# Optimization experiments

Measured on AMD Instinct MI355X. Metric: run time of the kernel, lower is better.

## Reference

```python
import jax, jax.numpy as jnp
import numpy as np

N = 20000   # nodes
E = 160000  # edges
IN = 16     # in_channels
H = 32      # hidden_channels
MID = 32    # edge-MLP hidden width


def setup_inputs() -> dict:
    key = jax.random.key(0)
    ks = jax.random.split(key, 18)
    s = 0.1  # param scale
    return {
        "x": jax.random.normal(ks[0], (N, IN), jnp.float32),
        "edge_index": jax.random.randint(ks[1], (2, E), 0, N, dtype=jnp.int64),
        "edge_weight": jax.random.uniform(ks[2], (E,), jnp.float32),
        # edge_net1: Linear(1,32) -> SiLU -> Linear(32, IN*H)
        "en1_w1": jax.random.normal(ks[3], (1, MID), jnp.float32) * s,
        "en1_b1": jax.random.normal(ks[4], (MID,), jnp.float32) * s,
        "en1_w2": jax.random.normal(ks[5], (MID, IN * H), jnp.float32) * s,
        "en1_b2": jax.random.normal(ks[6], (IN * H,), jnp.float32) * s,
        "root1": jax.random.normal(ks[7], (IN, H), jnp.float32) * s,
        "bias1": jax.random.normal(ks[8], (H,), jnp.float32) * s,
        # edge_net2: Linear(1,32) -> SiLU -> Linear(32, H*H)
        "en2_w1": jax.random.normal(ks[9], (1, MID), jnp.float32) * s,
        "en2_b1": jax.random.normal(ks[10], (MID,), jnp.float32) * s,
        "en2_w2": jax.random.normal(ks[11], (MID, H * H), jnp.float32) * s,
        "en2_b2": jax.random.normal(ks[12], (H * H,), jnp.float32) * s,
        "root2": jax.random.normal(ks[13], (H, H), jnp.float32) * s,
        "bias2": jax.random.normal(ks[14], (H,), jnp.float32) * s,
        "dec_w": jax.random.normal(ks[15], (H, 1), jnp.float32) * s,
        "dec_b": jax.random.normal(ks[16], (1,), jnp.float32) * s,
    }


def _nnconv(x, src, dst, inv_cnt, e, w1, b1, w2, b2, root, bias, cin, cout):
    # edge MLP -> per-edge [cin, cout] weight matrix
    h = jax.nn.silu(e @ w1 + b1)            # [E, MID]
    w = (h @ w2 + b2).reshape(-1, cin, cout)  # [E, cin, cout]
    msg = jnp.einsum('ei,eio->eo', x[src], w)  # per-edge matmul [E, cout]
    agg = jax.ops.segment_sum(msg, dst, num_segments=N) * inv_cnt  # scatter-mean
    return agg + x @ root + bias


def reference(x, edge_index, edge_weight,
              en1_w1, en1_b1, en1_w2, en1_b2, root1, bias1,
              en2_w1, en2_b1, en2_w2, en2_b2, root2, bias2,
              dec_w, dec_b):
    src, dst = edge_index[0], edge_index[1]
    e = edge_weight[:, None]  # [E, 1]
    cnt = jax.ops.segment_sum(jnp.ones((E,), x.dtype), dst, num_segments=N)
    inv_cnt = (1.0 / jnp.maximum(cnt, 1.0))[:, None]  # [N, 1]
    h = _nnconv(x, src, dst, inv_cnt, e, en1_w1, en1_b1, en1_w2, en1_b2, root1, bias1, IN, H)
    h = jax.nn.silu(h)
    h = _nnconv(h, src, dst, inv_cnt, e, en2_w1, en2_b1, en2_w2, en2_b2, root2, bias2, H, H)
    h = jax.nn.silu(h)
    out = h @ dec_w + dec_b  # [N, 1]
    return out[:, 0]
```

## Files before the change

### kernel.cpp

```cpp
#include <hip/hip_runtime.h>
#include <hip/hip_bf16.h>

#define NN 20000
#define EE 160000
#define HH 32
#define MIDD 32
#define NB 128
#define EPB 1250

typedef _Float16 f16x4 __attribute__((ext_vector_type(4)));
typedef _Float16 f16x8 __attribute__((ext_vector_type(8)));
typedef float f32x4 __attribute__((ext_vector_type(4)));

__device__ __forceinline__ float silu_f(float v) {
    return __fdividef(v, 1.0f + __expf(-v));
}

__device__ __forceinline__ void gload_lds_b32(const void* gsrc, void* ldst) {
    __builtin_amdgcn_global_load_lds(
        (const __attribute__((address_space(1))) void*)gsrc,
        (__attribute__((address_space(3))) void*)ldst, 4, 0, 0);
}

__global__ __launch_bounds__(256) void prep_kernel(
    const int* __restrict__ ei,
    const float* __restrict__ w2a, const float* __restrict__ b2a,
    const float* __restrict__ ra,
    const float* __restrict__ w2b, const float* __restrict__ b2b,
    const float* __restrict__ rb,
    const float* __restrict__ x,
    unsigned int* __restrict__ histG,
    _Float16* __restrict__ Wt1, _Float16* __restrict__ Wt2,
    _Float16* __restrict__ x16) {
    const int t = threadIdx.x;
    if (blockIdx.x < NB) {
        __shared__ unsigned int h2[NN / 2];
        for (int i = t; i < NN / 2; i += 256) h2[i] = 0u;
        __syncthreads();
        const int base = blockIdx.x * EPB;
        for (int e = base + t; e < base + EPB; e += 256) {
            int d = ei[EE + e];
            atomicAdd(&h2[d >> 1], 1u << ((d & 1) * 16));
        }
        __syncthreads();
        unsigned int* outp = histG + (size_t)blockIdx.x * NN;
        for (int n = t; n < NN; n += 256)
            outp[n] = (h2[n >> 1] >> ((n & 1) * 16)) & 0xFFFFu;
        return;
    }
    int idx = (blockIdx.x - NB) * 256 + t;
    if (idx < 17408) {
        int o = idx / 544, k = idx % 544;
        float v;
        if (k < 512) {
            int m = k & 31, i = k >> 5;
            v = w2a[m * 512 + i * 32 + o];
        } else if (k < 528) {
            v = b2a[(k - 512) * 32 + o];
        } else {
            v = ra[(k - 528) * 32 + o];
        }
        Wt1[o * 544 + k] = (_Float16)v;
    } else if (idx < 52224) {
        int j = idx - 17408;
        int o = j / 1088, k = j % 1088;
        float v;
        if (k < 1024) {
            int m = k & 31, i = k >> 5;
            v = w2b[m * 1024 + i * 32 + o];
        } else if (k < 1056) {
            v = b2b[(k - 1024) * 32 + o];
        } else {
            v = rb[(k - 1056) * 32 + o];
        }
        Wt2[o * 1088 + k] = (_Float16)v;
    } else if (idx < 52224 + NN * 16) {
        int j = idx - 52224;
        x16[j] = (_Float16)x[j];
    }
}

__global__ __launch_bounds__(256) void colscan_kernel(
    unsigned int* __restrict__ histG, int* __restrict__ cnt,
    float* __restrict__ invc) {
    const int n = blockIdx.x * 256 + threadIdx.x;
    if (n >= NN) return;
    unsigned int s = 0;
    #pragma unroll 4
    for (int b = 0; b < NB; ++b) {
        unsigned int v = histG[(size_t)b * NN + n];
        histG[(size_t)b * NN + n] = s;
        s += v;
    }
    cnt[n] = (int)s;
    invc[n] = 1.0f / fmaxf((float)s, 1.0f);
}

__global__ __launch_bounds__(1024) void scan_kernel(
    const int* __restrict__ cnt, int* __restrict__ off) {
    const int t = threadIdx.x;
    const int base = t * 20;
    __shared__ int wtot[16];

    int c[20];
    if (base + 20 <= NN) {
        const int4* p = (const int4*)(cnt + base);
        #pragma unroll
        for (int q = 0; q < 5; ++q) *(int4*)&c[4 * q] = p[q];
    } else {
        #pragma unroll
        for (int r = 0; r < 20; ++r) {
            int idx = base + r;
            c[r] = (idx < NN) ? cnt[idx] : 0;
        }
    }

    int loc[20];
    int s = 0;
    #pragma unroll
    for (int r = 0; r < 20; ++r) { loc[r] = s; s += c[r]; }

    const int lane = t & 63, wv = t >> 6;
    int incl = s;
    #pragma unroll
    for (int d2 = 1; d2 < 64; d2 <<= 1) {
        int u = __shfl_up(incl, d2);
        if (lane >= d2) incl += u;
    }
    if (lane == 63) wtot[wv] = incl;
    __syncthreads();
    int wbase = 0;
    for (int p2 = 0; p2 < wv; ++p2) wbase += wtot[p2];

    const int excl = wbase + incl - s;

    int o[20];
    #pragma unroll
    for (int r = 0; r < 20; ++r) o[r] = excl + loc[r];

    if (base + 20 <= NN) {
        #pragma unroll
        for (int q = 0; q < 5; ++q)
            ((int4*)(off + base))[q] = *(const int4*)&o[4 * q];
    } else {
        #pragma unroll
        for (int r = 0; r < 20; ++r) {
            int idx = base + r;
            if (idx < NN) off[idx] = o[r];
        }
    }
    if (t == 0) off[NN] = EE;
}

__global__ __launch_bounds__(256) void scatter2_kernel(
    const int* __restrict__ ei, const float* __restrict__ ewt,
    const int* __restrict__ off, const unsigned int* __restrict__ histG,
    int2* __restrict__ spair) {
    __shared__ unsigned int r2[NN / 2];
    const int t = threadIdx.x, b = blockIdx.x;
    for (int i = t; i < NN / 2; i += 256) r2[i] = 0u;
    __syncthreads();
    const int base = b * EPB;
    const unsigned int* hb = histG + (size_t)b * NN;
    for (int e = base + t; e < base + EPB; e += 256) {
        int d = ei[EE + e];
        unsigned int old = atomicAdd(&r2[d >> 1], 1u << ((d & 1) * 16));
        int rank = (int)((old >> ((d & 1) * 16)) & 0xFFFFu);
        int pos = off[d] + (int)hb[d] + rank;
        spair[pos] = make_int2(ei[e], __float_as_int(ewt[e]));
    }
}


template <int CIN, bool DECODE>
__global__ __launch_bounds__(512, 4) void fused_layer(
    const _Float16* __restrict__ xin16, const int* __restrict__ spair,
    const int* __restrict__ off, const float* __restrict__ invc,
    const float* __restrict__ w1, const float* __restrict__ b1,
    const _Float16* __restrict__ Wt, const float* __restrict__ bias,
    void* __restrict__ outp, const float* __restrict__ dw,
    const float* __restrict__ db) {
    constexpr int K = 34 * CIN;
    constexpr int LDK = K + 4;
    constexpr int steps = K / 32;
    constexpr int CAP = 192;
    constexpr int RPG = 128 / CIN;
    constexpr int LPR = CIN / 2;
    constexpr int NIH = CIN / 16;

    extern __shared__ char smem[];
    _Float16* Fl = (_Float16*)smem;
    char* poolb = smem + (size_t)16 * LDK * 2;
    int* Ps = (int*)poolb;
    _Float16* Xs = (_Float16*)(poolb + (2 * CAP + 64) * 4);
    _Float16* Hs = Xs + CAP * CIN;
    float* red = (float*)poolb;

    const int t = threadIdx.x;
    const int n0 = blockIdx.x * 16;
    const int lane = t & 63, w = t >> 6;
    const int col = lane & 15, g4 = (lane >> 4) * 4;

    const int E0 = off[n0], E1 = off[n0 + 16];
    const int L = E1 - E0;

    const int d0 = n0 + w * 2;
    const int e0l0 = off[d0] - E0;
    const int e1l0 = off[d0 + 1] - E0;
    const int e1l1 = off[d0 + 2] - E0;

    f32x4 aS[2][2][NIH];
    f32x4 a0[2][NIH];
    #pragma unroll
    for (int c = 0; c < 2; ++c) {
        #pragma unroll
        for (int mh = 0; mh < 2; ++mh)
            #pragma unroll
            for (int ih = 0; ih < NIH; ++ih) aS[c][mh][ih] = (f32x4){0.f, 0.f, 0.f, 0.f};
        #pragma unroll
        for (int ih = 0; ih < NIH; ++ih) a0[c][ih] = (f32x4){0.f, 0.f, 0.f, 0.f};
    }

    for (int base = 0; base < L; base += CAP) {
        const int Lc = (L - base < CAP) ? (L - base) : CAP;

        for (int c = w * 64; c < 2 * Lc; c += 512) {
            int gidx = 2 * (E0 + base) + c + lane;
            gidx = (gidx < 2 * EE) ? gidx : (2 * EE - 1);
            gload_lds_b32(spair + gidx, Ps + c);
        }
        __syncthreads();

        {
            const int G = (Lc + RPG - 1) / RPG;
            const int er = lane / LPR, ecp = lane % LPR;
            for (int p = w; p < G; p += 8) {
                int el = p * RPG + er; el = (el < Lc - 1) ? el : (Lc - 1);
                int sn = Ps[2 * el];
                gload_lds_b32(xin16 + (size_t)sn * CIN + 2 * ecp,
                              Xs + (size_t)p * RPG * CIN);
            }
        }
        for (int idx = t; idx < Lc * 32; idx += 512) {
            int e = idx >> 5, m = idx & 31;
            float ew = __int_as_float(Ps[2 * e + 1]);
            Hs[idx] = (_Float16)silu_f(fmaf(ew, w1[m], b1[m]));
        }
        __syncthreads();

        #pragma unroll
        for (int c = 0; c < 2; ++c) {
            int lo = ((c == 0) ? e0l0 : e1l0) - base;
            int hi = ((c == 0) ? e1l0 : e1l1) - base;
            lo = (lo < 0) ? 0 : lo;
            hi = (hi > Lc) ? Lc : hi;
            for (int ks = lo; ks < hi; ks += 32) {
                f16x8 bf[NIH];
                #pragma unroll
                for (int ih = 0; ih < NIH; ++ih)
                    #pragma unroll
                    for (int j = 0; j < 4; ++j) {
                        int k1 = ks + g4 + j, k2 = k1 + 16;
                        int c1 = (k1 < hi) ? k1 : (Lc - 1);
                        int c2 = (k2 < hi) ? k2 : (Lc - 1);
                        bf[ih][j]     = Xs[c1 * CIN + ih * 16 + col];
                        bf[ih][j + 4] = Xs[c2 * CIN + ih * 16 + col];
                    }
                f16x8 af[2];
                #pragma unroll
                for (int mh = 0; mh < 2; ++mh)
                    #pragma unroll
                    for (int j = 0; j < 4; ++j) {
                        int k1 = ks + g4 + j, k2 = k1 + 16;
                        _Float16 v1 = Hs[((k1 < hi) ? k1 : (Lc - 1)) * 32 + mh * 16 + col];
                        _Float16 v2 = Hs[((k2 < hi) ? k2 : (Lc - 1)) * 32 + mh * 16 + col];
                        af[mh][j]     = (k1 < hi) ? v1 : (_Float16)0;
                        af[mh][j + 4] = (k2 < hi) ? v2 : (_Float16)0;
                    }
                f16x8 ao;
                #pragma unroll
                for (int j = 0; j < 4; ++j) {
                    int k1 = ks + g4 + j, k2 = k1 + 16;
                    ao[j]     = (col == 0 && k1 < hi) ? (_Float16)1 : (_Float16)0;
                    ao[j + 4] = (col == 0 && k2 < hi) ? (_Float16)1 : (_Float16)0;
                }
                #pragma unroll
                for (int mh = 0; mh < 2; ++mh)
                    #pragma unroll
                    for (int ih = 0; ih < NIH; ++ih)
                        aS[c][mh][ih] = __builtin_amdgcn_mfma_f32_16x16x32_f16(
                            af[mh], bf[ih], aS[c][mh][ih], 0, 0, 0);
                #pragma unroll
                for (int ih = 0; ih < NIH; ++ih)
                    a0[c][ih] = __builtin_amdgcn_mfma_f32_16x16x32_f16(
                        ao, bf[ih], a0[c][ih], 0, 0, 0);
            }
        }
        if (base + CAP < L) __syncthreads();
    }

    #pragma unroll
    for (int c = 0; c < 2; ++c) {
        const int d = n0 + w * 2 + c;
        const float iv = invc[d];
        _Float16* Fr = Fl + (size_t)(w * 2 + c) * LDK;
        #pragma unroll
        for (int mh = 0; mh < 2; ++mh)
            #pragma unroll
            for (int ih = 0; ih < NIH; ++ih)
                #pragma unroll
                for (int r = 0; r < 4; ++r)
                    Fr[32 * (ih * 16 + col) + mh * 16 + g4 + r] =
                        (_Float16)(aS[c][mh][ih][r] * iv);
        if (g4 == 0) {
            #pragma unroll
            for (int ih = 0; ih < NIH; ++ih)
                Fr[32 * CIN + ih * 16 + col] = (_Float16)(a0[c][ih][0] * iv);
        }
        if (lane >= CIN && lane < 2 * CIN)
            Fr[32 * CIN + lane] = xin16[(size_t)d * CIN + (lane - CIN)];
    }
    __syncthreads();

    const int o16 = col, g = lane >> 4;

    const _Float16* Arow = Fl + (size_t)o16 * LDK + g * 4;
    const _Float16* B0 = Wt + (size_t)o16 * K + g * 4;
    const _Float16* B1 = Wt + (size_t)(o16 + 16) * K + g * 4;

    f32x4 acc0 = {0.f, 0.f, 0.f, 0.f};
    f32x4 acc1 = {0.f, 0.f, 0.f, 0.f};

    const int sb = (steps * w) >> 3;
    const int se = (steps * (w + 1)) >> 3;
    #pragma unroll 2
    for (int s = sb; s < se; ++s) {
        const int k0 = s * 32;
        f16x4 alo = *(const f16x4*)(Arow + k0);
        f16x4 ahi = *(const f16x4*)(Arow + k0 + 16);
        f16x4 b0l = *(const f16x4*)(B0 + k0);
        f16x4 b0h = *(const f16x4*)(B0 + k0 + 16);
        f16x4 b1l = *(const f16x4*)(B1 + k0);
        f16x4 b1h = *(const f16x4*)(B1 + k0 + 16);
        f16x8 a, bb0, bb1;
        #pragma unroll
        for (int j = 0; j < 4; ++j) {
            a[j] = alo[j];  a[j + 4] = ahi[j];
            bb0[j] = b0l[j]; bb0[j + 4] = b0h[j];
            bb1[j] = b1l[j]; bb1[j + 4] = b1h[j];
        }
        acc0 = __builtin_amdgcn_mfma_f32_16x16x32_f16(a, bb0, acc0, 0, 0, 0);
        acc1 = __builtin_amdgcn_mfma_f32_16x16x32_f16(a, bb1, acc1, 0, 0, 0);
    }

    if (w > 0) {
        float* rw = red + (w - 1) * 512;
        #pragma unroll
        for (int r = 0; r < 4; ++r) {
            rw[(g * 4 + r) * 32 + o16]      = acc0[r];
            rw[(g * 4 + r) * 32 + 16 + o16] = acc1[r];
        }
    }
    __syncthreads();
    if (w == 0) {
        #pragma unroll
        for (int r = 0; r < 4; ++r) {
            const int ro = (g * 4 + r) * 32 + o16;
            #pragma unroll
            for (int p = 0; p < 7; ++p) {
                acc0[r] += red[p * 512 + ro];
                acc1[r] += red[p * 512 + ro + 16];
            }
        }
        const float bb0 = bias[o16], bb1 = bias[o16 + 16];
        const int nrow = n0 + g * 4;
        if (!DECODE) {
            _Float16* op = (_Float16*)outp;
            #pragma unroll
            for (int r = 0; r < 4; ++r) {
                op[(size_t)(nrow + r) * 32 + o16]      = (_Float16)silu_f(acc0[r] + bb0);
                op[(size_t)(nrow + r) * 32 + 16 + o16] = (_Float16)silu_f(acc1[r] + bb1);
            }
        } else {
            float* op = (float*)outp;
            const float w0 = dw[o16], w1v = dw[o16 + 16];
            const float dbv = db[0];
            #pragma unroll
            for (int r = 0; r < 4; ++r) {
                float p = silu_f(acc0[r] + bb0) * w0 + silu_f(acc1[r] + bb1) * w1v;
                p += __shfl_xor(p, 1);
                p += __shfl_xor(p, 2);
                p += __shfl_xor(p, 4);
                p += __shfl_xor(p, 8);
                if (o16 == 0) op[nrow + r] = p + dbv;
            }
        }
    }
}


extern "C" void kernel_launch(void* const* d_in, const int* in_sizes, int n_in,
                              void* d_out, int out_size, void* d_ws, size_t ws_size,
                              hipStream_t stream) {
    const float* x      = (const float*)d_in[0];
    const int*   ei     = (const int*)d_in[1];
    const float* ew     = (const float*)d_in[2];
    const float* en1_w1 = (const float*)d_in[3];
    const float* en1_b1 = (const float*)d_in[4];
    const float* en1_w2 = (const float*)d_in[5];
    const float* en1_b2 = (const float*)d_in[6];
    const float* root1  = (const float*)d_in[7];
    const float* bias1  = (const float*)d_in[8];
    const float* en2_w1 = (const float*)d_in[9];
    const float* en2_b1 = (const float*)d_in[10];
    const float* en2_w2 = (const float*)d_in[11];
    const float* en2_b2 = (const float*)d_in[12];
    const float* root2  = (const float*)d_in[13];
    const float* bias2  = (const float*)d_in[14];
    const float* dec_w  = (const float*)d_in[15];
    const float* dec_b  = (const float*)d_in[16];
    float* out = (float*)d_out;
    (void)in_sizes; (void)n_in; (void)out_size; (void)ws_size;

    char* wp = (char*)d_ws;
    auto alloc = [&](size_t bytes) {
        char* p = wp;
        wp += (bytes + 255) & ~(size_t)255;
        return p;
    };
    unsigned int* histG = (unsigned int*)alloc((size_t)NB * NN * 4);
    int*      cnt   = (int*)alloc((size_t)NN * 4);
    int*      off   = (int*)alloc((size_t)(NN + 1) * 4);
    float*    invc  = (float*)alloc((size_t)NN * 4);
    int2*     spair = (int2*)alloc((size_t)EE * 8);
    _Float16* h1h   = (_Float16*)alloc((size_t)NN * 32 * 2);
    _Float16* x16   = (_Float16*)alloc((size_t)NN * 16 * 2);
    _Float16* Wt1   = (_Float16*)alloc((size_t)17408 * 2);
    _Float16* Wt2   = (_Float16*)alloc((size_t)34816 * 2);

    const int build_blocks = (52224 + NN * 16 + 255) / 256;
    prep_kernel<<<NB + build_blocks, 256, 0, stream>>>(
        ei, en1_w2, en1_b2, root1, en2_w2, en2_b2, root2, x,
        histG, Wt1, Wt2, x16);
    colscan_kernel<<<(NN + 255) / 256, 256, 0, stream>>>(histG, cnt, invc);
    scan_kernel<<<1, 1024, 0, stream>>>(cnt, off);
    scatter2_kernel<<<NB, 256, 0, stream>>>(ei, ew, off, histG, spair);

    auto f1 = fused_layer<16, false>;
    auto f2 = fused_layer<32, true>;
    (void)hipFuncSetAttribute((const void*)f1,
                              hipFuncAttributeMaxDynamicSharedMemorySize, 163840);
    (void)hipFuncSetAttribute((const void*)f2,
                              hipFuncAttributeMaxDynamicSharedMemorySize, 163840);

    const size_t lds1 = (size_t)16 * (34 * 16 + 4) * 2 + (448 * 4 + 192 * 16 * 2 + 192 * 64);
    const size_t lds2 = (size_t)16 * (34 * 32 + 4) * 2 + (448 * 4 + 192 * 32 * 2 + 192 * 64);

    fused_layer<16, false><<<NN / 16, 512, lds1, stream>>>(
        x16, (const int*)spair, off, invc, en1_w1, en1_b1, Wt1, bias1, h1h,
        nullptr, nullptr);
    fused_layer<32, true><<<NN / 16, 512, lds2, stream>>>(
        h1h, (const int*)spair, off, invc, en2_w1, en2_b1, Wt2, bias2, out,
        dec_w, dec_b);
}
```

Before: 97.23 us.

## Merge column and offset scans, drop LDS edge staging, parallelize final reduction

Folds the single-block prefix scan into the column-scan kernel with a last-block-done atomic counter, which removes one kernel launch; prep_kernel resets the counter. The fused layers no longer stage the sorted (src, weight) pairs into LDS behind a barrier and instead read them straight from global memory. The edge-MLP first-layer weights are now loaded once per thread. The cross-wave reduction and epilogue are spread over all eight waves instead of being done by wave 0 alone. In exchange the code adds a threadfence and atomic in the scan path, and issues redundant global reads of the edge pairs.

```diff
diff --git a/kernel.cpp b/kernel.cpp
--- a/kernel.cpp
+++ b/kernel.cpp
@@ -31,7 +31,7 @@
     const float* __restrict__ x,
     unsigned int* __restrict__ histG,
     _Float16* __restrict__ Wt1, _Float16* __restrict__ Wt2,
-    _Float16* __restrict__ x16) {
+    _Float16* __restrict__ x16, int* __restrict__ flag) {
     const int t = threadIdx.x;
     if (blockIdx.x < NB) {
         __shared__ unsigned int h2[NN / 2];
@@ -48,6 +48,7 @@
             outp[n] = (h2[n >> 1] >> ((n & 1) * 16)) & 0xFFFFu;
         return;
     }
+    if (blockIdx.x == NB && t == 0) *flag = 0;
     int idx = (blockIdx.x - NB) * 256 + t;
     if (idx < 17408) {
         int o = idx / 544, k = idx % 544;
@@ -80,46 +81,39 @@
     }
 }
 
-__global__ __launch_bounds__(256) void colscan_kernel(
+__global__ __launch_bounds__(256) void colscan_scan_kernel(
     unsigned int* __restrict__ histG, int* __restrict__ cnt,
-    float* __restrict__ invc) {
+    float* __restrict__ invc, int* __restrict__ off, int* __restrict__ flag) {
     const int n = blockIdx.x * 256 + threadIdx.x;
-    if (n >= NN) return;
-    unsigned int s = 0;
-    #pragma unroll 4
-    for (int b = 0; b < NB; ++b) {
-        unsigned int v = histG[(size_t)b * NN + n];
-        histG[(size_t)b * NN + n] = s;
-        s += v;
-    }
-    cnt[n] = (int)s;
-    invc[n] = 1.0f / fmaxf((float)s, 1.0f);
-}
-
-__global__ __launch_bounds__(1024) void scan_kernel(
-    const int* __restrict__ cnt, int* __restrict__ off) {
+    if (n < NN) {
+        unsigned int s = 0;
+        #pragma unroll 4
+        for (int b = 0; b < NB; ++b) {
+            unsigned int v = histG[(size_t)b * NN + n];
+            histG[(size_t)b * NN + n] = s;
+            s += v;
+        }
+        cnt[n] = (int)s;
+        invc[n] = 1.0f / fmaxf((float)s, 1.0f);
+    }
+    __threadfence();
+    __shared__ int isLast;
+    __shared__ int wtot[4];
+    if (threadIdx.x == 0)
+        isLast = (atomicAdd(flag, 1) == (int)gridDim.x - 1) ? 1 : 0;
+    __syncthreads();
+    if (!isLast) return;
+
     const int t = threadIdx.x;
-    const int base = t * 20;
-    __shared__ int wtot[16];
-
-    int c[20];
-    if (base + 20 <= NN) {
-        const int4* p = (const int4*)(cnt + base);
-        #pragma unroll
-        for (int q = 0; q < 5; ++q) *(int4*)&c[4 * q] = p[q];
-    } else {
-        #pragma unroll
-        for (int r = 0; r < 20; ++r) {
-            int idx = base + r;
-            c[r] = (idx < NN) ? cnt[idx] : 0;
-        }
-    }
-
-    int loc[20];
+    const int base = t * 80;
     int s = 0;
-    #pragma unroll
-    for (int r = 0; r < 20; ++r) { loc[r] = s; s += c[r]; }
-
+    if (base + 80 <= NN) {
+        #pragma unroll
+        for (int q = 0; q < 20; ++q) {
+            int4 v = ((const int4*)(cnt + base))[q];
+            s += v.x + v.y + v.z + v.w;
+        }
+    }
     const int lane = t & 63, wv = t >> 6;
     int incl = s;
     #pragma unroll
@@ -131,22 +125,18 @@
     __syncthreads();
     int wbase = 0;
     for (int p2 = 0; p2 < wv; ++p2) wbase += wtot[p2];
-
-    const int excl = wbase + incl - s;
-
-    int o[20];
-    #pragma unroll
-    for (int r = 0; r < 20; ++r) o[r] = excl + loc[r];
-
-    if (base + 20 <= NN) {
-        #pragma unroll
-        for (int q = 0; q < 5; ++q)
-            ((int4*)(off + base))[q] = *(const int4*)&o[4 * q];
-    } else {
-        #pragma unroll
-        for (int r = 0; r < 20; ++r) {
-            int idx = base + r;
-            if (idx < NN) off[idx] = o[r];
+    int running = wbase + incl - s;
+    if (base + 80 <= NN) {
+        #pragma unroll
+        for (int q = 0; q < 20; ++q) {
+            int4 v = ((const int4*)(cnt + base))[q];
+            int4 o;
+            o.x = running;
+            o.y = running + v.x;
+            o.z = o.y + v.y;
+            o.w = o.z + v.z;
+            ((int4*)(off + base))[q] = o;
+            running = o.w + v.w;
         }
     }
     if (t == 0) off[NN] = EE;
@@ -174,7 +164,7 @@
 
 template <int CIN, bool DECODE>
 __global__ __launch_bounds__(512, 4) void fused_layer(
-    const _Float16* __restrict__ xin16, const int* __restrict__ spair,
+    const _Float16* __restrict__ xin16, const int2* __restrict__ spair,
     const int* __restrict__ off, const float* __restrict__ invc,
     const float* __restrict__ w1, const float* __restrict__ b1,
     const _Float16* __restrict__ Wt, const float* __restrict__ bias,
@@ -191,8 +181,7 @@
     extern __shared__ char smem[];
     _Float16* Fl = (_Float16*)smem;
     char* poolb = smem + (size_t)16 * LDK * 2;
-    int* Ps = (int*)poolb;
-    _Float16* Xs = (_Float16*)(poolb + (2 * CAP + 64) * 4);
+    _Float16* Xs = (_Float16*)poolb;
     _Float16* Hs = Xs + CAP * CIN;
     float* red = (float*)poolb;
 
@@ -221,30 +210,26 @@
         for (int ih = 0; ih < NIH; ++ih) a0[c][ih] = (f32x4){0.f, 0.f, 0.f, 0.f};
     }
 
+    const float w1v = w1[t & 31];
+    const float b1v = b1[t & 31];
+
     for (int base = 0; base < L; base += CAP) {
         const int Lc = (L - base < CAP) ? (L - base) : CAP;
-
-        for (int c = w * 64; c < 2 * Lc; c += 512) {
-            int gidx = 2 * (E0 + base) + c + lane;
-            gidx = (gidx < 2 * EE) ? gidx : (2 * EE - 1);
-            gload_lds_b32(spair + gidx, Ps + c);
-        }
-        __syncthreads();
 
         {
             const int G = (Lc + RPG - 1) / RPG;
             const int er = lane / LPR, ecp = lane % LPR;
             for (int p = w; p < G; p += 8) {
                 int el = p * RPG + er; el = (el < Lc - 1) ? el : (Lc - 1);
-                int sn = Ps[2 * el];
+                int sn = spair[E0 + base + el].x;
                 gload_lds_b32(xin16 + (size_t)sn * CIN + 2 * ecp,
                               Xs + (size_t)p * RPG * CIN);
             }
         }
         for (int idx = t; idx < Lc * 32; idx += 512) {
-            int e = idx >> 5, m = idx & 31;
-            float ew = __int_as_float(Ps[2 * e + 1]);
-            Hs[idx] = (_Float16)silu_f(fmaf(ew, w1[m], b1[m]));
+            int e = idx >> 5;
+            float ew = __int_as_float(spair[E0 + base + e].y);
+            Hs[idx] = (_Float16)silu_f(fmaf(ew, w1v, b1v));
         }
         __syncthreads();
 
@@ -353,8 +338,8 @@
         acc1 = __builtin_amdgcn_mfma_f32_16x16x32_f16(a, bb1, acc1, 0, 0, 0);
     }
 
-    if (w > 0) {
-        float* rw = red + (w - 1) * 512;
+    {
+        float* rw = red + w * 512;
         #pragma unroll
         for (int r = 0; r < 4; ++r) {
             rw[(g * 4 + r) * 32 + o16]      = acc0[r];
@@ -362,38 +347,25 @@
         }
     }
     __syncthreads();
-    if (w == 0) {
-        #pragma unroll
-        for (int r = 0; r < 4; ++r) {
-            const int ro = (g * 4 + r) * 32 + o16;
-            #pragma unroll
-            for (int p = 0; p < 7; ++p) {
-                acc0[r] += red[p * 512 + ro];
-                acc1[r] += red[p * 512 + ro + 16];
-            }
-        }
-        const float bb0 = bias[o16], bb1 = bias[o16 + 16];
-        const int nrow = n0 + g * 4;
+
+    {
+        const int rsub = 2 * w + (lane >> 5);
+        const int outc = lane & 31;
+        float v = 0.f;
+        #pragma unroll
+        for (int p = 0; p < 8; ++p) v += red[p * 512 + rsub * 32 + outc];
+        v += bias[outc];
+        const int nrow = n0 + rsub;
         if (!DECODE) {
-            _Float16* op = (_Float16*)outp;
-            #pragma unroll
-            for (int r = 0; r < 4; ++r) {
-                op[(size_t)(nrow + r) * 32 + o16]      = (_Float16)silu_f(acc0[r] + bb0);
-                op[(size_t)(nrow + r) * 32 + 16 + o16] = (_Float16)silu_f(acc1[r] + bb1);
-            }
+            ((_Float16*)outp)[(size_t)nrow * 32 + outc] = (_Float16)silu_f(v);
         } else {
-            float* op = (float*)outp;
-            const float w0 = dw[o16], w1v = dw[o16 + 16];
-            const float dbv = db[0];
-            #pragma unroll
-            for (int r = 0; r < 4; ++r) {
-                float p = silu_f(acc0[r] + bb0) * w0 + silu_f(acc1[r] + bb1) * w1v;
-                p += __shfl_xor(p, 1);
-                p += __shfl_xor(p, 2);
-                p += __shfl_xor(p, 4);
-                p += __shfl_xor(p, 8);
-                if (o16 == 0) op[nrow + r] = p + dbv;
-            }
+            float pd = silu_f(v) * dw[outc];
+            pd += __shfl_xor(pd, 1);
+            pd += __shfl_xor(pd, 2);
+            pd += __shfl_xor(pd, 4);
+            pd += __shfl_xor(pd, 8);
+            pd += __shfl_xor(pd, 16);
+            if (outc == 0) ((float*)outp)[nrow] = pd + db[0];
         }
     }
 }
@@ -437,13 +409,14 @@
     _Float16* x16   = (_Float16*)alloc((size_t)NN * 16 * 2);
     _Float16* Wt1   = (_Float16*)alloc((size_t)17408 * 2);
     _Float16* Wt2   = (_Float16*)alloc((size_t)34816 * 2);
+    int*      flag  = (int*)alloc(256);
 
     const int build_blocks = (52224 + NN * 16 + 255) / 256;
     prep_kernel<<<NB + build_blocks, 256, 0, stream>>>(
         ei, en1_w2, en1_b2, root1, en2_w2, en2_b2, root2, x,
-        histG, Wt1, Wt2, x16);
-    colscan_kernel<<<(NN + 255) / 256, 256, 0, stream>>>(histG, cnt, invc);
-    scan_kernel<<<1, 1024, 0, stream>>>(cnt, off);
+        histG, Wt1, Wt2, x16, flag);
+    colscan_scan_kernel<<<(NN + 255) / 256, 256, 0, stream>>>(
+        histG, cnt, invc, off, flag);
     scatter2_kernel<<<NB, 256, 0, stream>>>(ei, ew, off, histG, spair);
 
     auto f1 = fused_layer<16, false>;
@@ -453,13 +426,13 @@
     (void)hipFuncSetAttribute((const void*)f2,
                               hipFuncAttributeMaxDynamicSharedMemorySize, 163840);
 
-    const size_t lds1 = (size_t)16 * (34 * 16 + 4) * 2 + (448 * 4 + 192 * 16 * 2 + 192 * 64);
-    const size_t lds2 = (size_t)16 * (34 * 32 + 4) * 2 + (448 * 4 + 192 * 32 * 2 + 192 * 64);
+    const size_t lds1 = (size_t)16 * (34 * 16 + 4) * 2 + (192 * 16 * 2 + 192 * 64);
+    const size_t lds2 = (size_t)16 * (34 * 32 + 4) * 2 + (192 * 32 * 2 + 192 * 64);
 
     fused_layer<16, false><<<NN / 16, 512, lds1, stream>>>(
-        x16, (const int*)spair, off, invc, en1_w1, en1_b1, Wt1, bias1, h1h,
+        x16, spair, off, invc, en1_w1, en1_b1, Wt1, bias1, h1h,
         nullptr, nullptr);
     fused_layer<32, true><<<NN / 16, 512, lds2, stream>>>(
-        h1h, (const int*)spair, off, invc, en2_w1, en2_b1, Wt2, bias2, out,
+        h1h, spair, off, invc, en2_w1, en2_b1, Wt2, bias2, out,
         dec_w, dec_b);
 }
```

Result: slower. 108.7 us (+11.8%).
